# Kernel tuning notes

Hardware: AMD Instinct MI355X
Metric: run time of the kernel (lower is better)

Reference implementation:

```python
import jax, jax.numpy as jnp
import numpy as np

DN = ('NCHW', 'OIHW', 'NCHW')

def _conv(x, w, pad):
    return jax.lax.conv_general_dilated(x, w, window_strides=(1, 1),
                                        padding=[(pad, pad), (pad, pad)],
                                        dimension_numbers=DN)

def _channel_shuffle(x, perm):
    # x: [B, C, H, W]; perm: [C, H*W] per-channel spatial permutation
    B, C, H, W = x.shape
    y = jnp.take_along_axis(x.reshape(B, C, H * W), perm[None, :, :], axis=2)
    return y.reshape(B, C, H, W)

def setup_inputs() -> dict:
    key = jax.random.key(0)
    k = jax.random.split(key, 6)
    B, Cin, H, W = 32, 1024, 28, 28
    P1, P2, P3 = 256, 256, 1024
    HW = H * W
    x = jax.random.normal(k[0], (B, Cin, H, W), dtype=jnp.float32)
    w1 = jax.random.normal(k[1], (P1, Cin, 1, 1), dtype=jnp.float32) * np.sqrt(2.0 / Cin)
    wd = jax.random.normal(k[2], (P2, P1, 3, 3), dtype=jnp.float32) * np.sqrt(2.0 / (P1 * 9))
    w3 = jax.random.normal(k[3], (P3, P2, 1, 1), dtype=jnp.float32) * np.sqrt(2.0 / P2)
    perm_dconv = jax.vmap(lambda kk: jax.random.permutation(kk, HW))(
        jax.random.split(k[4], P1)).astype(jnp.int32)
    perm_res = jax.vmap(lambda kk: jax.random.permutation(kk, HW))(
        jax.random.split(k[5], Cin)).astype(jnp.int32)
    return {"x": x, "w1": w1, "wd": wd, "w3": w3,
            "perm_dconv": perm_dconv, "perm_res": perm_res}

def reference(x, w1, wd, w3, perm_dconv, perm_res):
    # conv1 (1x1) + relu
    y = jax.nn.relu(_conv(x, w1, 0))
    # Dconv_shuffle: per-channel spatial shuffle then 3x3 conv (pad=1), relu
    y = _channel_shuffle(y, perm_dconv)
    y = jax.nn.relu(_conv(y, wd, 1))
    # conv3 (1x1)
    y = _conv(y, w3, 0)
    # residual: per-channel spatially shuffled input, add, relu
    res = _channel_shuffle(x, perm_res)
    return jax.nn.relu(y + res)
```

## Files before the change

kernel.cpp:

```cpp
#include <hip/hip_runtime.h>
#include <hip/hip_bf16.h>

#define BATCH 32
#define CIN   1024
#define HW    784
#define WIMG  28
#define PADW  30
#define PADHW 900
#define P1    256
#define P2    256
#define P3    1024
#define NFLAT (BATCH * HW)

typedef __attribute__((ext_vector_type(8))) short bfrag_t;
typedef __attribute__((ext_vector_type(8))) unsigned short usvec8;
typedef __attribute__((ext_vector_type(4))) unsigned short usvec4;
typedef __attribute__((ext_vector_type(4))) float accvec_t;

static __device__ __forceinline__ unsigned short f2bf(float f) {
    union { __hip_bfloat16 h; unsigned short u; } cv;
    cv.h = __float2bfloat16(f);
    return cv.u;
}
static __device__ __forceinline__ float bf2f(unsigned short u) {
    union { float f; unsigned int i; } cv;
    cv.i = ((unsigned int)u) << 16;
    return cv.f;
}

#define GLDS16(g, l) __builtin_amdgcn_global_load_lds(                      \
        (const __attribute__((address_space(1))) void*)(g),                 \
        (__attribute__((address_space(3))) void*)(l), 16, 0, 0)

#define RAW_BARRIER() do {                         \
        __builtin_amdgcn_sched_barrier(0);         \
        __builtin_amdgcn_s_barrier();              \
        __builtin_amdgcn_sched_barrier(0);         \
    } while (0)
#define WAITCNT_VM(N) do {                                        \
        asm volatile("s_waitcnt vmcnt(" #N ")" ::: "memory");     \
        __builtin_amdgcn_sched_barrier(0);                        \
    } while (0)

__global__ __launch_bounds__(256) void permT_kernel(const int* __restrict__ perm,
                                                    int* __restrict__ permT) {
    int p = blockIdx.x, c = threadIdx.x;
    permT[p * P1 + c] = perm[c * HW + p];
}

__global__ __launch_bounds__(256) void pack_weights_kernel(
        const float* __restrict__ w1, const float* __restrict__ wd,
        const float* __restrict__ w3, unsigned short* __restrict__ w1b,
        unsigned short* __restrict__ wdb, unsigned short* __restrict__ w3b) {
    int i = blockIdx.x * 256 + threadIdx.x;
    if (i < 262144) w1b[i] = f2bf(w1[i]);
    int i2 = i - 262144;
    if (i2 >= 0 && i2 < 262144) w3b[i2] = f2bf(w3[i2]);
    int i3 = i - 524288;
    if (i3 >= 0 && i3 < 589824) {
        int m = i3 / 2304, rem = i3 - m * 2304;
        int k = rem / 9, r = rem - k * 9;
        wdb[((size_t)r * P2 + m) * P1 + k] = f2bf(wd[i3]);
    }
}

__global__ __launch_bounds__(256) void transpose_x_kernel(const float* __restrict__ x,
                                                          unsigned short* __restrict__ xt) {
    __shared__ __align__(16) unsigned short T[64 * 72];
    const int c0 = blockIdx.x * 64;
    const int n0 = blockIdx.y * 64;
    const int t  = threadIdx.x;
    const int f  = t & 15;
    const int cg = t >> 4;
    const int n  = n0 + f * 4;
    const int b  = n / HW, hw = n - b * HW;
    const float* xb = x + ((size_t)b * CIN + c0 + cg * 4) * HW + hw;
    float4 v0 = *(const float4*)&xb[0];
    float4 v1 = *(const float4*)&xb[HW];
    float4 v2 = *(const float4*)&xb[2 * HW];
    float4 v3 = *(const float4*)&xb[3 * HW];
    const float* vr[4] = {(const float*)&v0, (const float*)&v1,
                          (const float*)&v2, (const float*)&v3};
#pragma unroll
    for (int q = 0; q < 4; ++q) {
        usvec4 w;
        w[0] = f2bf(vr[0][q]);
        w[1] = f2bf(vr[1][q]);
        w[2] = f2bf(vr[2][q]);
        w[3] = f2bf(vr[3][q]);
        *(usvec4*)&T[(f * 4 + q) * 72 + cg * 4] = w;
    }
    __syncthreads();
#pragma unroll
    for (int it = 0; it < 2; ++it) {
        int idx  = it * 256 + t;
        int hw_l = idx >> 3, cgo = idx & 7;
        usvec8 w = *(const usvec8*)&T[hw_l * 72 + cgo * 8];
        *(usvec8*)&xt[(size_t)(n0 + hw_l) * CIN + c0 + cgo * 8] = w;
    }
}

__global__ __launch_bounds__(256) void res_shuffle_kernel(const float* __restrict__ x,
                                                          const int* __restrict__ perm_res,
                                                          unsigned short* __restrict__ res) {
    __shared__ float Lx[8 * 788];
    const int g0 = blockIdx.x * 8;
    const int t = threadIdx.x;
#pragma unroll
    for (int it = 0; it < 7; ++it) {
        int chunk = it * 256 + t;
        if (chunk < 1568) {
            int r = chunk / 196, off = (chunk - r * 196) * 4;
            float4 v = *(const float4*)&x[(size_t)(g0 + r) * HW + off];
            *(float4*)&Lx[r * 788 + off] = v;
        }
    }
    __syncthreads();
    const int q0 = t & 63;
#pragma unroll
    for (int rp = 0; rp < 2; ++rp) {
        int r = rp * 4 + (t >> 6);
        int g = g0 + r;
        int m = g & (CIN - 1);
        const int* pr = perm_res + (size_t)m * HW;
#pragma unroll
        for (int it = 0; it < 13; ++it) {
            int q = it * 64 + q0;
            if (q < HW) {
                int pv = pr[q];
                res[(size_t)g * HW + q] = f2bf(Lx[r * 788 + pv]);
            }
        }
    }
}

__global__ __launch_bounds__(512) void shuffle_pad_kernel(const unsigned short* __restrict__ y1c,
                                                          const int* __restrict__ permT,
                                                          unsigned short* __restrict__ y1sp) {
    __shared__ unsigned short Ly[32 * 800];
    const int b  = blockIdx.x >> 3;
    const int c0 = (blockIdx.x & 7) * 32;
    const int t = threadIdx.x;
#pragma unroll
    for (int it = 0; it < 7; ++it) {
        int chunk = it * 512 + t;
        if (chunk < 3136) {
            int c = chunk / 98, off8 = (chunk - c * 98) * 8;
            usvec8 v = *(const usvec8*)&y1c[((size_t)(b * P1 + c0 + c)) * HW + off8];
            *(usvec8*)&Ly[c * 800 + off8] = v;
        }
    }
    __syncthreads();
    const int pc = t & 31, pi = t >> 5;
    unsigned short* yb = y1sp + (size_t)b * PADHW * P1 + c0 + pc;
#pragma unroll 7
    for (int it = 0; it < 49; ++it) {
        int p = it * 16 + pi;
        int pv = permT[p * P1 + c0 + pc];
        unsigned short val = Ly[pc * 800 + pv];
        int ph = p / WIMG, pw = p - ph * WIMG;
        yb[(size_t)((ph + 1) * PADW + pw + 1) * P1] = val;
    }
}


__global__ __launch_bounds__(256) void conv1_kernel(const unsigned short* __restrict__ xt,
                                                    const unsigned short* __restrict__ w1b,
                                                    unsigned short* __restrict__ y1c) {
    __shared__ __align__(16) unsigned short As[2 * 128 * 64];
    __shared__ __align__(16) unsigned short Bs[2 * 128 * 64];
    const int m0 = blockIdx.x * 128;
    const int n0 = blockIdx.y * 128;
    const int t = threadIdx.x;
    const int lane = t & 63, wave = t >> 6;
    const int l15 = lane & 15, quad = lane >> 4;
    const int wm = wave & 1, wn = wave >> 1;
    const int grow = lane >> 3;
    const int gsw  = ((lane & 7) ^ grow) << 3;
    const unsigned short* Asrc[4];
    const unsigned short* Bsrc[4];
    int ldso[4];
#pragma unroll
    for (int j = 0; j < 4; ++j) {
        int q = wave * 4 + j;
        int row = (q << 3) + grow;
        Asrc[j] = w1b + (size_t)(m0 + row) * CIN + gsw;
        Bsrc[j] = xt + (size_t)(n0 + row) * CIN + gsw;
        ldso[j] = q * 512;
    }
    const int coff0 = ((quad)     ^ (l15 & 7)) << 3;
    const int coff1 = ((quad + 4) ^ (l15 & 7)) << 3;

    accvec_t acc[4][4];
    const accvec_t zero = {0.f, 0.f, 0.f, 0.f};
#pragma unroll
    for (int i = 0; i < 4; ++i)
#pragma unroll
        for (int j = 0; j < 4; ++j) acc[i][j] = zero;

    auto stage = [&](int cur, int k0) {
        unsigned short* Ab = As + cur * 8192;
        unsigned short* Bb = Bs + cur * 8192;
#pragma unroll
        for (int j = 0; j < 4; ++j) {
            GLDS16(Asrc[j] + k0, Ab + ldso[j]);
            GLDS16(Bsrc[j] + k0, Bb + ldso[j]);
        }
    };
    auto compute = [&](int cur) {
        const unsigned short* Ab = As + cur * 8192;
        const unsigned short* Bb = Bs + cur * 8192;
        bfrag_t af[4], bfr[4];
#pragma unroll
        for (int i = 0; i < 4; ++i) {
            af[i]  = *(const bfrag_t*)&Ab[(wm * 64 + i * 16 + l15) * 64 + coff0];
            bfr[i] = *(const bfrag_t*)&Bb[(wn * 64 + i * 16 + l15) * 64 + coff0];
        }
#pragma unroll
        for (int im = 0; im < 4; ++im)
#pragma unroll
            for (int in = 0; in < 4; ++in)
                acc[im][in] = __builtin_amdgcn_mfma_f32_16x16x32_bf16(af[im], bfr[in], acc[im][in], 0, 0, 0);
#pragma unroll
        for (int i = 0; i < 4; ++i) {
            af[i]  = *(const bfrag_t*)&Ab[(wm * 64 + i * 16 + l15) * 64 + coff1];
            bfr[i] = *(const bfrag_t*)&Bb[(wn * 64 + i * 16 + l15) * 64 + coff1];
        }
#pragma unroll
        for (int im = 0; im < 4; ++im)
#pragma unroll
            for (int in = 0; in < 4; ++in)
                acc[im][in] = __builtin_amdgcn_mfma_f32_16x16x32_bf16(af[im], bfr[in], acc[im][in], 0, 0, 0);
    };

    stage(0, 0);
    for (int s = 0; s < 16; s += 2) {
        stage(1, (s + 1) << 6);
        WAITCNT_VM(8);
        RAW_BARRIER();
        compute(0);
        RAW_BARRIER();
        if (s + 2 < 16) { stage(0, (s + 2) << 6); WAITCNT_VM(8); }
        else            { WAITCNT_VM(0); }
        RAW_BARRIER();
        compute(1);
        RAW_BARRIER();
    }
#pragma unroll
    for (int in = 0; in < 4; ++in) {
        const int n = n0 + wn * 64 + in * 16 + l15;
        const int b = n / HW, hw = n - b * HW;
#pragma unroll
        for (int im = 0; im < 4; ++im) {
#pragma unroll
            for (int r = 0; r < 4; ++r) {
                const int m = m0 + wm * 64 + im * 16 + (quad << 2) + r;
                float v = acc[im][in][r];
                v = v > 0.f ? v : 0.f;
                y1c[((size_t)(b * P1 + m)) * HW + hw] = f2bf(v);
            }
        }
    }
}

__global__ __launch_bounds__(256) void dconv_kernel(const unsigned short* __restrict__ y1sp,
                                                    const unsigned short* __restrict__ wdb,
                                                    unsigned short* __restrict__ y2t) {
    __shared__ __align__(16) unsigned short As[2 * 128 * 64];
    __shared__ __align__(16) unsigned short Bs[2 * 128 * 64];
    const int m0 = blockIdx.x * 128;
    const int n0 = blockIdx.y * 128;
    const int t = threadIdx.x;
    const int lane = t & 63, wave = t >> 6;
    const int l15 = lane & 15, quad = lane >> 4;
    const int wm = wave & 1, wn = wave >> 1;
    const int grow = lane >> 3;
    const int gsw  = ((lane & 7) ^ grow) << 3;
    const unsigned short* Asrc[4];
    const unsigned short* Bsrc[4];
    int ldso[4];
#pragma unroll
    for (int j = 0; j < 4; ++j) {
        int q = wave * 4 + j;
        int row = (q << 3) + grow;
        Asrc[j] = wdb + (size_t)(m0 + row) * P1 + gsw;
        int n = n0 + row;
        int b = n / HW, hw = n - b * HW;
        int h = hw / WIMG, w = hw - h * WIMG;
        Bsrc[j] = y1sp + ((size_t)b * PADHW + h * PADW + w) * P1 + gsw;
        ldso[j] = q * 512;
    }
    const int coff0 = ((quad)     ^ (l15 & 7)) << 3;
    const int coff1 = ((quad + 4) ^ (l15 & 7)) << 3;

    accvec_t acc[4][4];
    const accvec_t zero = {0.f, 0.f, 0.f, 0.f};
#pragma unroll
    for (int i = 0; i < 4; ++i)
#pragma unroll
        for (int j = 0; j < 4; ++j) acc[i][j] = zero;

    auto stage = [&](int cur, int s) {
        const int r  = s >> 2;
        const int k0 = (s & 3) << 6;
        const int kh = r / 3, kw = r - kh * 3;
        const size_t aoff = (size_t)r * (P1 * P2) + k0;
        const int    toff = (kh * PADW + kw) * P1 + k0;
        unsigned short* Ab = As + cur * 8192;
        unsigned short* Bb = Bs + cur * 8192;
#pragma unroll
        for (int j = 0; j < 4; ++j) {
            GLDS16(Asrc[j] + aoff, Ab + ldso[j]);
            GLDS16(Bsrc[j] + toff, Bb + ldso[j]);
        }
    };
    auto compute = [&](int cur) {
        const unsigned short* Ab = As + cur * 8192;
        const unsigned short* Bb = Bs + cur * 8192;
        bfrag_t af[4], bfr[4];
#pragma unroll
        for (int i = 0; i < 4; ++i) {
            af[i]  = *(const bfrag_t*)&Ab[(wm * 64 + i * 16 + l15) * 64 + coff0];
            bfr[i] = *(const bfrag_t*)&Bb[(wn * 64 + i * 16 + l15) * 64 + coff0];
        }
#pragma unroll
        for (int im = 0; im < 4; ++im)
#pragma unroll
            for (int in = 0; in < 4; ++in)
                acc[im][in] = __builtin_amdgcn_mfma_f32_16x16x32_bf16(bfr[in], af[im], acc[im][in], 0, 0, 0);
#pragma unroll
        for (int i = 0; i < 4; ++i) {
            af[i]  = *(const bfrag_t*)&Ab[(wm * 64 + i * 16 + l15) * 64 + coff1];
            bfr[i] = *(const bfrag_t*)&Bb[(wn * 64 + i * 16 + l15) * 64 + coff1];
        }
#pragma unroll
        for (int im = 0; im < 4; ++im)
#pragma unroll
            for (int in = 0; in < 4; ++in)
                acc[im][in] = __builtin_amdgcn_mfma_f32_16x16x32_bf16(bfr[in], af[im], acc[im][in], 0, 0, 0);
    };

    stage(0, 0);
    for (int s = 0; s < 36; s += 2) {
        stage(1, s + 1);
        WAITCNT_VM(8);
        RAW_BARRIER();
        compute(0);
        RAW_BARRIER();
        if (s + 2 < 36) { stage(0, s + 2); WAITCNT_VM(8); }
        else            { WAITCNT_VM(0); }
        RAW_BARRIER();
        compute(1);
        RAW_BARRIER();
    }
#pragma unroll
    for (int im = 0; im < 4; ++im) {
        const int m = m0 + wm * 64 + im * 16 + l15;
#pragma unroll
        for (int in = 0; in < 4; ++in) {
#pragma unroll
            for (int r = 0; r < 4; ++r) {
                const int n = n0 + wn * 64 + in * 16 + (quad << 2) + r;
                float v = acc[im][in][r];
                v = v > 0.f ? v : 0.f;
                y2t[(size_t)n * P2 + m] = f2bf(v);
            }
        }
    }
}

__global__ __launch_bounds__(256) void conv3_kernel(const unsigned short* __restrict__ y2t,
                                                    const unsigned short* __restrict__ w3b,
                                                    const unsigned short* __restrict__ res,
                                                    float* __restrict__ out) {
    __shared__ __align__(16) unsigned short SMEM[16384];
    unsigned short* AsB = SMEM;
    unsigned short* BsB = SMEM + 8192;
    float* Obuf = (float*)SMEM;

    const int m0 = blockIdx.x * 128;
    const int n0 = blockIdx.y * 128;
    const int t = threadIdx.x;
    const int lane = t & 63, wave = t >> 6;
    const int l15 = lane & 15, quad = lane >> 4;
    const int wm = wave & 1, wn = wave >> 1;
    const int srow = lane >> 2, c8 = (lane & 3) << 3;
    const int row0 = wave * 32 + srow, row1 = row0 + 16;

    const unsigned short* a0 = w3b + (size_t)(m0 + row0) * P2 + c8;
    const unsigned short* a1 = w3b + (size_t)(m0 + row1) * P2 + c8;
    const unsigned short* b0 = y2t + (size_t)(n0 + row0) * P2 + c8;
    const unsigned short* b1 = y2t + (size_t)(n0 + row1) * P2 + c8;
    const int o0 = (wave * 2 + 0) * 512, o1 = (wave * 2 + 1) * 512;

    const int erow = t >> 3, eseg = t & 7;
    const int n_e  = n0 + eseg * 16;
    const int b_e  = n_e / HW;
    const int hw_e = n_e - b_e * HW;
    const size_t ebase0 = ((size_t)(b_e * P3 + m0 + erow)) * HW + hw_e;

    usvec8 rsA = *(const usvec8*)&res[ebase0];
    usvec8 rsB = *(const usvec8*)&res[ebase0 + 8];

    accvec_t acc[4][4];
    const accvec_t zero = {0.f, 0.f, 0.f, 0.f};
#pragma unroll
    for (int i = 0; i < 4; ++i)
#pragma unroll
        for (int j = 0; j < 4; ++j) acc[i][j] = zero;

    auto stage = [&](int cur, int k0) {
        unsigned short* Ab = AsB + cur * 4096;
        unsigned short* Bb = BsB + cur * 4096;
        GLDS16(a0 + k0, Ab + o0);
        GLDS16(a1 + k0, Ab + o1);
        GLDS16(b0 + k0, Bb + o0);
        GLDS16(b1 + k0, Bb + o1);
    };
    auto compute = [&](int cur) {
        const unsigned short* Ab = AsB + cur * 4096;
        const unsigned short* Bb = BsB + cur * 4096;
        bfrag_t af[4], bfr[4];
#pragma unroll
        for (int i = 0; i < 4; ++i) {
            af[i]  = *(const bfrag_t*)&Ab[(wm * 64 + i * 16 + l15) * 32 + (quad << 3)];
            bfr[i] = *(const bfrag_t*)&Bb[(wn * 64 + i * 16 + l15) * 32 + (quad << 3)];
        }
#pragma unroll
        for (int im = 0; im < 4; ++im)
#pragma unroll
            for (int in = 0; in < 4; ++in)
                acc[im][in] = __builtin_amdgcn_mfma_f32_16x16x32_bf16(af[im], bfr[in], acc[im][in], 0, 0, 0);
    };

    stage(0, 0);
    for (int s = 0; s < 8; s += 2) {
        stage(1, (s + 1) << 5);
        WAITCNT_VM(4);
        RAW_BARRIER();
        compute(0);
        RAW_BARRIER();
        if (s + 2 < 8) { stage(0, (s + 2) << 5); WAITCNT_VM(4); }
        else           { WAITCNT_VM(0); }
        RAW_BARRIER();
        compute(1);
        RAW_BARRIER();
    }

#pragma unroll
    for (int c = 0; c < 4; ++c) {
        if (wm == (c >> 1)) {
            const int imb = (c & 1) * 2;
#pragma unroll
            for (int i2 = 0; i2 < 2; ++i2)
#pragma unroll
                for (int in = 0; in < 4; ++in)
#pragma unroll
                    for (int r = 0; r < 4; ++r)
                        Obuf[(i2 * 16 + (quad << 2) + r) * 132 + wn * 64 + in * 16 + l15] =
                            acc[imb + i2][in][r];
        }
        __syncthreads();
        usvec8 nxA = rsA, nxB = rsB;
        if (c < 3) {
            const size_t nb = ebase0 + (size_t)(c + 1) * 32 * HW;
            nxA = *(const usvec8*)&res[nb];
            nxB = *(const usvec8*)&res[nb + 8];
        }
        {
            const size_t base = ebase0 + (size_t)c * 32 * HW;
            float ov[16];
#pragma unroll
            for (int q4 = 0; q4 < 4; ++q4) {
                float4 v = *(const float4*)&Obuf[erow * 132 + eseg * 16 + q4 * 4];
                ov[q4 * 4 + 0] = v.x; ov[q4 * 4 + 1] = v.y;
                ov[q4 * 4 + 2] = v.z; ov[q4 * 4 + 3] = v.w;
            }
#pragma unroll
            for (int q4 = 0; q4 < 4; ++q4) {
                float4 w;
                float e0, e1, e2, e3;
                const int j = q4 * 4;
                e0 = ov[j + 0] + bf2f((unsigned short)(j + 0 < 8 ? rsA[j + 0] : rsB[j + 0 - 8]));
                e1 = ov[j + 1] + bf2f((unsigned short)(j + 1 < 8 ? rsA[j + 1] : rsB[j + 1 - 8]));
                e2 = ov[j + 2] + bf2f((unsigned short)(j + 2 < 8 ? rsA[j + 2] : rsB[j + 2 - 8]));
                e3 = ov[j + 3] + bf2f((unsigned short)(j + 3 < 8 ? rsA[j + 3] : rsB[j + 3 - 8]));
                w.x = e0 > 0.f ? e0 : 0.f;
                w.y = e1 > 0.f ? e1 : 0.f;
                w.z = e2 > 0.f ? e2 : 0.f;
                w.w = e3 > 0.f ? e3 : 0.f;
                *(float4*)&out[base + q4 * 4] = w;
            }
        }
        rsA = nxA; rsB = nxB;
        if (c < 3) __syncthreads();
    }
}

extern "C" void kernel_launch(void* const* d_in, const int* in_sizes, int n_in,
                              void* d_out, int out_size, void* d_ws, size_t ws_size,
                              hipStream_t stream) {
    const float* x      = (const float*)d_in[0];
    const float* w1     = (const float*)d_in[1];
    const float* wd     = (const float*)d_in[2];
    const float* w3     = (const float*)d_in[3];
    const int*   perm_d = (const int*)d_in[4];
    const int*   perm_r = (const int*)d_in[5];
    float*       out    = (float*)d_out;

    char* ws = (char*)d_ws;
    unsigned short* y1sp  = (unsigned short*)(ws + 0);
    unsigned short* y2t   = (unsigned short*)(ws + 14745600);
    int*            permT = (int*)(ws + 27590656);
    unsigned short* w1b   = (unsigned short*)(ws + 28393472);
    unsigned short* wdb   = (unsigned short*)(ws + 28917760);
    unsigned short* w3b   = (unsigned short*)(ws + 30097408);
    unsigned short* xt    = (unsigned short*)(ws + 30621696);
    unsigned short* resb  = xt;
    unsigned short* y1c   = y2t;

    hipMemsetAsync(y1sp, 0, (size_t)BATCH * PADHW * P1 * sizeof(unsigned short), stream);
    permT_kernel<<<dim3(HW), dim3(256), 0, stream>>>(perm_d, permT);
    pack_weights_kernel<<<dim3(4352), dim3(256), 0, stream>>>(w1, wd, w3, w1b, wdb, w3b);
    transpose_x_kernel<<<dim3(CIN / 64, NFLAT / 64), dim3(256), 0, stream>>>(x, xt);

    conv1_kernel<<<dim3(P1 / 128, NFLAT / 128), dim3(256), 0, stream>>>(xt, w1b, y1c);
    res_shuffle_kernel<<<dim3(BATCH * CIN / 8), dim3(256), 0, stream>>>(x, perm_r, resb);
    shuffle_pad_kernel<<<dim3(BATCH * 8), dim3(512), 0, stream>>>(y1c, permT, y1sp);
    dconv_kernel<<<dim3(P2 / 128, NFLAT / 128), dim3(256), 0, stream>>>(y1sp, wdb, y2t);
    conv3_kernel<<<dim3(P3 / 128, NFLAT / 128), dim3(256), 0, stream>>>(y2t, w3b, resb, out);
}
```

Baseline: 351.1 us.

## Merge prep kernels into one launch and co-schedule residual shuffle with dconv

Combines the x transpose, weight packing, perm transpose and padded-buffer zeroing (replacing the memset) into one heterogeneous prep kernel dispatched by block index. The residual shuffle work is appended as extra blocks of the 3x3 conv kernel so it fills idle CUs during the under-occupied dconv grid. This removes several launches and their serialization gaps. The cost is a larger shared-memory footprint for the merged kernel and some branch-dependent scheduling.

```diff
diff --git a/kernel.cpp b/kernel.cpp
--- a/kernel.cpp
+++ b/kernel.cpp
@@ -42,95 +42,65 @@
         __builtin_amdgcn_sched_barrier(0);                        \
     } while (0)
 
-__global__ __launch_bounds__(256) void permT_kernel(const int* __restrict__ perm,
-                                                    int* __restrict__ permT) {
-    int p = blockIdx.x, c = threadIdx.x;
-    permT[p * P1 + c] = perm[c * HW + p];
-}
-
-__global__ __launch_bounds__(256) void pack_weights_kernel(
+__global__ __launch_bounds__(256) void prep_kernel(
+        const float* __restrict__ x, unsigned short* __restrict__ xt,
         const float* __restrict__ w1, const float* __restrict__ wd,
         const float* __restrict__ w3, unsigned short* __restrict__ w1b,
-        unsigned short* __restrict__ wdb, unsigned short* __restrict__ w3b) {
-    int i = blockIdx.x * 256 + threadIdx.x;
-    if (i < 262144) w1b[i] = f2bf(w1[i]);
-    int i2 = i - 262144;
-    if (i2 >= 0 && i2 < 262144) w3b[i2] = f2bf(w3[i2]);
-    int i3 = i - 524288;
-    if (i3 >= 0 && i3 < 589824) {
-        int m = i3 / 2304, rem = i3 - m * 2304;
-        int k = rem / 9, r = rem - k * 9;
-        wdb[((size_t)r * P2 + m) * P1 + k] = f2bf(wd[i3]);
-    }
-}
-
-__global__ __launch_bounds__(256) void transpose_x_kernel(const float* __restrict__ x,
-                                                          unsigned short* __restrict__ xt) {
+        unsigned short* __restrict__ wdb, unsigned short* __restrict__ w3b,
+        const int* __restrict__ perm, int* __restrict__ permT,
+        unsigned short* __restrict__ y1sp) {
     __shared__ __align__(16) unsigned short T[64 * 72];
-    const int c0 = blockIdx.x * 64;
-    const int n0 = blockIdx.y * 64;
-    const int t  = threadIdx.x;
-    const int f  = t & 15;
-    const int cg = t >> 4;
-    const int n  = n0 + f * 4;
-    const int b  = n / HW, hw = n - b * HW;
-    const float* xb = x + ((size_t)b * CIN + c0 + cg * 4) * HW + hw;
-    float4 v0 = *(const float4*)&xb[0];
-    float4 v1 = *(const float4*)&xb[HW];
-    float4 v2 = *(const float4*)&xb[2 * HW];
-    float4 v3 = *(const float4*)&xb[3 * HW];
-    const float* vr[4] = {(const float*)&v0, (const float*)&v1,
-                          (const float*)&v2, (const float*)&v3};
-#pragma unroll
-    for (int q = 0; q < 4; ++q) {
-        usvec4 w;
-        w[0] = f2bf(vr[0][q]);
-        w[1] = f2bf(vr[1][q]);
-        w[2] = f2bf(vr[2][q]);
-        w[3] = f2bf(vr[3][q]);
-        *(usvec4*)&T[(f * 4 + q) * 72 + cg * 4] = w;
-    }
-    __syncthreads();
-#pragma unroll
-    for (int it = 0; it < 2; ++it) {
-        int idx  = it * 256 + t;
-        int hw_l = idx >> 3, cgo = idx & 7;
-        usvec8 w = *(const usvec8*)&T[hw_l * 72 + cgo * 8];
-        *(usvec8*)&xt[(size_t)(n0 + hw_l) * CIN + c0 + cgo * 8] = w;
-    }
-}
-
-__global__ __launch_bounds__(256) void res_shuffle_kernel(const float* __restrict__ x,
-                                                          const int* __restrict__ perm_res,
-                                                          unsigned short* __restrict__ res) {
-    __shared__ float Lx[8 * 788];
-    const int g0 = blockIdx.x * 8;
-    const int t = threadIdx.x;
-#pragma unroll
-    for (int it = 0; it < 7; ++it) {
-        int chunk = it * 256 + t;
-        if (chunk < 1568) {
-            int r = chunk / 196, off = (chunk - r * 196) * 4;
-            float4 v = *(const float4*)&x[(size_t)(g0 + r) * HW + off];
-            *(float4*)&Lx[r * 788 + off] = v;
-        }
-    }
-    __syncthreads();
-    const int q0 = t & 63;
-#pragma unroll
-    for (int rp = 0; rp < 2; ++rp) {
-        int r = rp * 4 + (t >> 6);
-        int g = g0 + r;
-        int m = g & (CIN - 1);
-        const int* pr = perm_res + (size_t)m * HW;
-#pragma unroll
-        for (int it = 0; it < 13; ++it) {
-            int q = it * 64 + q0;
-            if (q < HW) {
-                int pv = pr[q];
-                res[(size_t)g * HW + q] = f2bf(Lx[r * 788 + pv]);
-            }
-        }
+    const int bid = blockIdx.x;
+    const int t   = threadIdx.x;
+    if (bid < 6272) {
+        const int c0 = (bid & 15) * 64;
+        const int n0 = (bid >> 4) * 64;
+        const int f  = t & 15;
+        const int cg = t >> 4;
+        const int n  = n0 + f * 4;
+        const int b  = n / HW, hw = n - b * HW;
+        const float* xb = x + ((size_t)b * CIN + c0 + cg * 4) * HW + hw;
+        float4 v0 = *(const float4*)&xb[0];
+        float4 v1 = *(const float4*)&xb[HW];
+        float4 v2 = *(const float4*)&xb[2 * HW];
+        float4 v3 = *(const float4*)&xb[3 * HW];
+        const float* vr[4] = {(const float*)&v0, (const float*)&v1,
+                              (const float*)&v2, (const float*)&v3};
+#pragma unroll
+        for (int q = 0; q < 4; ++q) {
+            usvec4 w;
+            w[0] = f2bf(vr[0][q]);
+            w[1] = f2bf(vr[1][q]);
+            w[2] = f2bf(vr[2][q]);
+            w[3] = f2bf(vr[3][q]);
+            *(usvec4*)&T[(f * 4 + q) * 72 + cg * 4] = w;
+        }
+        __syncthreads();
+#pragma unroll
+        for (int it = 0; it < 2; ++it) {
+            int idx  = it * 256 + t;
+            int hw_l = idx >> 3, cgo = idx & 7;
+            usvec8 w = *(const usvec8*)&T[hw_l * 72 + cgo * 8];
+            *(usvec8*)&xt[(size_t)(n0 + hw_l) * CIN + c0 + cgo * 8] = w;
+        }
+    } else if (bid < 10624) {
+        int i = (bid - 6272) * 256 + t;
+        if (i < 262144) w1b[i] = f2bf(w1[i]);
+        int i2 = i - 262144;
+        if (i2 >= 0 && i2 < 262144) w3b[i2] = f2bf(w3[i2]);
+        int i3 = i - 524288;
+        if (i3 >= 0 && i3 < 589824) {
+            int m = i3 / 2304, rem = i3 - m * 2304;
+            int k = rem / 9, r = rem - k * 9;
+            wdb[((size_t)r * P2 + m) * P1 + k] = f2bf(wd[i3]);
+        }
+    } else if (bid < 11408) {
+        int p = bid - 10624;
+        permT[p * P1 + t] = perm[t * HW + p];
+    } else {
+        int z = bid - 11408;
+        usvec8 zv = {0, 0, 0, 0, 0, 0, 0, 0};
+        *(usvec8*)&y1sp[((size_t)z * 256 + t) * 8] = zv;
     }
 }
 
@@ -162,7 +132,6 @@
         yb[(size_t)((ph + 1) * PADW + pw + 1) * P1] = val;
     }
 }
-
 
 __global__ __launch_bounds__(256) void conv1_kernel(const unsigned short* __restrict__ xt,
                                                     const unsigned short* __restrict__ w1b,
@@ -263,14 +232,50 @@
     }
 }
 
-__global__ __launch_bounds__(256) void dconv_kernel(const unsigned short* __restrict__ y1sp,
-                                                    const unsigned short* __restrict__ wdb,
-                                                    unsigned short* __restrict__ y2t) {
-    __shared__ __align__(16) unsigned short As[2 * 128 * 64];
-    __shared__ __align__(16) unsigned short Bs[2 * 128 * 64];
-    const int m0 = blockIdx.x * 128;
-    const int n0 = blockIdx.y * 128;
+__global__ __launch_bounds__(256) void dconv_res_kernel(const unsigned short* __restrict__ y1sp,
+                                                        const unsigned short* __restrict__ wdb,
+                                                        unsigned short* __restrict__ y2t,
+                                                        const float* __restrict__ x,
+                                                        const int* __restrict__ perm_res,
+                                                        unsigned short* __restrict__ res) {
+    __shared__ __align__(16) unsigned char SM[65536];
+    const int bid = blockIdx.x;
     const int t = threadIdx.x;
+    if (bid >= 392) {
+        float* Lx = (float*)SM;
+        const int g0 = (bid - 392) * 8;
+#pragma unroll
+        for (int it = 0; it < 7; ++it) {
+            int chunk = it * 256 + t;
+            if (chunk < 1568) {
+                int r = chunk / 196, off = (chunk - r * 196) * 4;
+                float4 v = *(const float4*)&x[(size_t)(g0 + r) * HW + off];
+                *(float4*)&Lx[r * 788 + off] = v;
+            }
+        }
+        __syncthreads();
+        const int q0 = t & 63;
+#pragma unroll
+        for (int rp = 0; rp < 2; ++rp) {
+            int r = rp * 4 + (t >> 6);
+            int g = g0 + r;
+            int m = g & (CIN - 1);
+            const int* pr = perm_res + (size_t)m * HW;
+#pragma unroll
+            for (int it = 0; it < 13; ++it) {
+                int q = it * 64 + q0;
+                if (q < HW) {
+                    int pv = pr[q];
+                    res[(size_t)g * HW + q] = f2bf(Lx[r * 788 + pv]);
+                }
+            }
+        }
+        return;
+    }
+    unsigned short* As = (unsigned short*)SM;
+    unsigned short* Bs = (unsigned short*)(SM + 32768);
+    const int m0 = (bid & 1) * 128;
+    const int n0 = (bid >> 1) * 128;
     const int lane = t & 63, wave = t >> 6;
     const int l15 = lane & 15, quad = lane >> 4;
     const int wm = wave & 1, wn = wave >> 1;
@@ -519,14 +524,12 @@
     unsigned short* resb  = xt;
     unsigned short* y1c   = y2t;
 
-    hipMemsetAsync(y1sp, 0, (size_t)BATCH * PADHW * P1 * sizeof(unsigned short), stream);
-    permT_kernel<<<dim3(HW), dim3(256), 0, stream>>>(perm_d, permT);
-    pack_weights_kernel<<<dim3(4352), dim3(256), 0, stream>>>(w1, wd, w3, w1b, wdb, w3b);
-    transpose_x_kernel<<<dim3(CIN / 64, NFLAT / 64), dim3(256), 0, stream>>>(x, xt);
-
+    prep_kernel<<<dim3(15008), dim3(256), 0, stream>>>(x, xt, w1, wd, w3,
+                                                       w1b, wdb, w3b,
+                                                       perm_d, permT, y1sp);
     conv1_kernel<<<dim3(P1 / 128, NFLAT / 128), dim3(256), 0, stream>>>(xt, w1b, y1c);
-    res_shuffle_kernel<<<dim3(BATCH * CIN / 8), dim3(256), 0, stream>>>(x, perm_r, resb);
     shuffle_pad_kernel<<<dim3(BATCH * 8), dim3(512), 0, stream>>>(y1c, permT, y1sp);
-    dconv_kernel<<<dim3(P2 / 128, NFLAT / 128), dim3(256), 0, stream>>>(y1sp, wdb, y2t);
+    dconv_res_kernel<<<dim3(392 + BATCH * CIN / 8), dim3(256), 0, stream>>>(
+        y1sp, wdb, y2t, x, perm_r, resb);
     conv3_kernel<<<dim3(P3 / 128, NFLAT / 128), dim3(256), 0, stream>>>(y2t, w3b, resb, out);
 }
```

After: 331.5 us. -5.6%, faster.
